# Kernel optimization log

Hardware: AMD Instinct MI355X
Metric: run time of the kernel (lower is better)

The kernel has to match this reference:

```python
import jax, jax.numpy as jnp
import numpy as np

S, B, DIM = 1024, 4, 768
N_EXPERTS = 8
# hidden_dim = 256 * ceil(int(2*4*dim/3)/256) = 2048 for dim=768
HID = 2048


def setup_inputs() -> dict:
    key = jax.random.key(0)
    ks = jax.random.split(key, 6)
    scale = 0.02
    return {
        "hidden_states": jax.random.normal(ks[0], (S, B, DIM), dtype=jnp.float32),
        "router_w": jax.random.normal(ks[1], (DIM, N_EXPERTS), dtype=jnp.float32) * scale,
        "router_b": jnp.zeros((N_EXPERTS,), dtype=jnp.float32),
        "w1": jax.random.normal(ks[2], (N_EXPERTS, DIM, HID), dtype=jnp.float32) * scale,
        "w2": jax.random.normal(ks[3], (N_EXPERTS, DIM, HID), dtype=jnp.float32) * scale,
        "w3": jax.random.normal(ks[4], (N_EXPERTS, HID, DIM), dtype=jnp.float32) * scale,
    }


def reference(hidden_states, router_w, router_b, w1, w2, w3):
    s, b, h = hidden_states.shape
    # top-1 router
    route = jax.nn.softmax(hidden_states @ router_w + router_b, axis=2)  # [s,b,E]
    max_prob = jnp.max(route, axis=2).reshape(-1, 1)   # [T,1]
    max_ind = jnp.argmax(route, axis=2).reshape(-1)    # [T]
    x = hidden_states.reshape(-1, h)                   # [T,d]

    out = jnp.zeros_like(x)
    # fixed small loop over experts; masked dispatch (tokens not routed to e
    # are zeroed so they contribute nothing)
    for e in range(N_EXPERTS):
        mask = (max_ind == e)[:, None]                 # [T,1]
        xe = jnp.where(mask, x, 0.0)
        oe = (jax.nn.silu(xe @ w1[e]) * (xe @ w2[e])) @ w3[e]
        out = out + jnp.where(mask, oe, 0.0)

    # original stores expert outputs in a bf16 buffer before the prob combine
    out = out.astype(jnp.bfloat16) * max_prob          # bf16 * f32 -> f32
    return out.reshape(s, b, h)
```

## Files before the change

kernel.cpp:

```cpp
#include <hip/hip_runtime.h>


#define T_TOK 4096
#define DIM   768
#define HID   2048
#define NE    8
#define ECAP  1024

#define KB1 24
#define NB1 128
#define KB2 64
#define NB2 48
#define MBC 64

typedef _Float16 f16x8 __attribute__((ext_vector_type(8)));
typedef float    f32x4 __attribute__((ext_vector_type(4)));

__device__ __forceinline__ float bf16_rne(float v) {
    unsigned u = __float_as_uint(v);
    unsigned r = (u + 0x7fffu + ((u >> 16) & 1u)) & 0xffff0000u;
    return __uint_as_float(r);
}

__global__ void moe_init_kernel(int* __restrict__ counts) {
    if (threadIdx.x < NE) counts[threadIdx.x] = 0;
}

__global__ __launch_bounds__(256) void moe_convert_kernel(
    const float* __restrict__ w1, const float* __restrict__ w2,
    const float* __restrict__ w3, _Float16* __restrict__ w1s,
    _Float16* __restrict__ w2s, _Float16* __restrict__ w3s)
{
    const int bid = blockIdx.x;
    const float* src; _Float16* dst; int N, KBc, ngrp, kgrp;
    if (bid < 1536) {
        const int e = bid / 192, tile = bid % 192;
        src = w1 + (size_t)e * DIM * HID; dst = w1s + (size_t)e * NB1 * KB1 * 512;
        N = HID; KBc = KB1; ngrp = tile & 15; kgrp = tile >> 4;
    } else if (bid < 3072) {
        const int r = bid - 1536, e = r / 192, tile = r % 192;
        src = w2 + (size_t)e * DIM * HID; dst = w2s + (size_t)e * NB1 * KB1 * 512;
        N = HID; KBc = KB1; ngrp = tile & 15; kgrp = tile >> 4;
    } else {
        const int r = bid - 3072, e = r / 192, tile = r % 192;
        src = w3 + (size_t)e * HID * DIM; dst = w3s + (size_t)e * NB2 * KB2 * 512;
        N = DIM; KBc = KB2; ngrp = tile % 6; kgrp = tile / 6;
    }

    __shared__ float Lt[64 * 130];
    const int t  = threadIdx.x;
    const int c4 = (t & 31) * 4;
    const int r0 = (t >> 5) * 8;
    const float* p = src + (size_t)(kgrp * 64 + r0) * N + ngrp * 128 + c4;
    float4 v[8];
#pragma unroll
    for (int j = 0; j < 8; ++j) v[j] = *(const float4*)(p + (size_t)j * N);
#pragma unroll
    for (int j = 0; j < 8; ++j) {
        float* row = &Lt[(r0 + j) * 130 + c4];
        *(float2*)(row)     = make_float2(v[j].x, v[j].y);
        *(float2*)(row + 2) = make_float2(v[j].z, v[j].w);
    }
    __syncthreads();

    const int l = t & 63, w = t >> 6;
    const int fr = l & 15, fq = l >> 4;
#pragma unroll
    for (int i = 0; i < 4; ++i) {
        const int cell = w * 4 + i;
        const int kbl = cell >> 3, nbl = cell & 7;
        f16x8 h;
#pragma unroll
        for (int j = 0; j < 8; ++j)
            h[j] = (_Float16)Lt[(kbl * 32 + fq * 8 + j) * 130 + nbl * 16 + fr];
        const int nb = ngrp * 8 + nbl, kb = kgrp * 2 + kbl;
        *(f16x8*)(dst + ((size_t)nb * KBc + kb) * 512 + l * 8) = h;
    }
}

__global__ __launch_bounds__(256) void moe_router_kernel(
    const float* __restrict__ X, const float* __restrict__ rw,
    const float* __restrict__ rb, float* __restrict__ probs,
    int* __restrict__ counts, int* __restrict__ lists)
{
    const int t    = blockIdx.x * 4 + (threadIdx.x >> 6);
    const int lane = threadIdx.x & 63;
    const float* x = X + (size_t)t * DIM;

    float xv[12];
#pragma unroll
    for (int j = 0; j < 12; ++j) xv[j] = x[lane + j * 64];

    double lg[NE];
#pragma unroll
    for (int e = 0; e < NE; ++e) {
        double s = 0.0;
#pragma unroll
        for (int j = 0; j < 12; ++j)
            s += (double)xv[j] * (double)rw[(lane + j * 64) * NE + e];
#pragma unroll
        for (int off = 32; off >= 1; off >>= 1) s += __shfl_xor(s, off, 64);
        lg[e] = s + (double)rb[e];
    }

    if (lane == 0) {
        double m = lg[0]; int mi = 0;
#pragma unroll
        for (int e = 1; e < NE; ++e)
            if (lg[e] > m) { m = lg[e]; mi = e; }
        float sum = 0.f;
#pragma unroll
        for (int e = 0; e < NE; ++e) sum += expf((float)(lg[e] - m));
        probs[t] = 1.0f / sum;
        int pos = atomicAdd(&counts[mi], 1);
        lists[mi * T_TOK + pos] = t;
    }
}

__global__ __launch_bounds__(256) void moe_gather_kernel(
    const float* __restrict__ X, const int* __restrict__ lists,
    const int* __restrict__ counts, _Float16* __restrict__ Ag)
{
    const int e = blockIdx.z;
    int cnt = counts[e]; if (cnt > ECAP) cnt = ECAP;
    const int mgrp = blockIdx.y;
    if (mgrp * 64 >= ((cnt + 63) & ~63)) return;
    const int t = threadIdx.x, w = t >> 6, l = t & 63;
    const int mb = mgrp * 4 + w;
    const int m  = mb * 16 + (l & 15);
    const bool valid = (m < cnt);
    const int tok = valid ? lists[e * T_TOK + m] : 0;
    const float* xr = X + (size_t)tok * DIM + (l >> 4) * 8;
#pragma unroll
    for (int i = 0; i < 4; ++i) {
        const int kb = blockIdx.x * 4 + i;
        float4 a = make_float4(0.f, 0.f, 0.f, 0.f), b = a;
        if (valid) {
            a = *(const float4*)(xr + kb * 32);
            b = *(const float4*)(xr + kb * 32 + 4);
        }
        f16x8 h;
        h[0] = (_Float16)a.x; h[1] = (_Float16)a.y; h[2] = (_Float16)a.z; h[3] = (_Float16)a.w;
        h[4] = (_Float16)b.x; h[5] = (_Float16)b.y; h[6] = (_Float16)b.z; h[7] = (_Float16)b.w;
        *(f16x8*)(Ag + ((size_t)(e * MBC + mb) * KB1 + kb) * 512 + l * 8) = h;
    }
}

__global__ __launch_bounds__(256, 3) void moe_gemm1_kernel(
    const _Float16* __restrict__ Ag, const _Float16* __restrict__ w1s,
    const _Float16* __restrict__ w2s, const int* __restrict__ counts,
    _Float16* __restrict__ Hs)
{
    const int e = blockIdx.z;
    int cnt = counts[e]; if (cnt > ECAP) cnt = ECAP;
    const int by = blockIdx.y, bx = blockIdx.x;
    if (by * 128 >= cnt) return;
    const int t = threadIdx.x, w = t >> 6, l = t & 63;
    const int wm = w & 1, wn = w >> 1;

    const _Float16* Ab  = Ag + ((size_t)((e * MBC + by * 8 + wm * 4) * KB1)) * 512 + l * 8;
    const int nb0 = e * NB1 + bx * 4 + wn * 2;
    const _Float16* B1b = w1s + ((size_t)nb0 * KB1) * 512 + l * 8;
    const _Float16* B2b = w2s + ((size_t)nb0 * KB1) * 512 + l * 8;

    f32x4 acc1[4][2], acc2[4][2];
    const f32x4 zero = {0.f, 0.f, 0.f, 0.f};
#pragma unroll
    for (int i = 0; i < 4; ++i)
#pragma unroll
        for (int j = 0; j < 2; ++j) { acc1[i][j] = zero; acc2[i][j] = zero; }

    f16x8 a0[4], p0[2], q0[2], a1[4], p1[2], q1[2];

    auto LD = [&](f16x8* a, f16x8* p, f16x8* q, int kb) {
#pragma unroll
        for (int i = 0; i < 4; ++i)
            a[i] = *(const f16x8*)(Ab + ((size_t)(i * KB1 + kb)) * 512);
#pragma unroll
        for (int j = 0; j < 2; ++j) {
            p[j] = *(const f16x8*)(B1b + ((size_t)(j * KB1 + kb)) * 512);
            q[j] = *(const f16x8*)(B2b + ((size_t)(j * KB1 + kb)) * 512);
        }
    };
    auto FM = [&](const f16x8* a, const f16x8* p, const f16x8* q) {
#pragma unroll
        for (int i = 0; i < 4; ++i)
#pragma unroll
            for (int j = 0; j < 2; ++j) {
                acc1[i][j] = __builtin_amdgcn_mfma_f32_16x16x32_f16(a[i], p[j], acc1[i][j], 0, 0, 0);
                acc2[i][j] = __builtin_amdgcn_mfma_f32_16x16x32_f16(a[i], q[j], acc2[i][j], 0, 0, 0);
            }
    };

    LD(a0, p0, q0, 0);
    int kb = 0;
    for (; kb + 2 < KB1; kb += 2) {
        LD(a1, p1, q1, kb + 1);
        FM(a0, p0, q0);
        LD(a0, p0, q0, kb + 2);
        FM(a1, p1, q1);
    }
    LD(a1, p1, q1, kb + 1);
    FM(a0, p0, q0);
    FM(a1, p1, q1);

    __shared__ _Float16 Ep[4][64 * 40];
    const int fq = l >> 4, fr = l & 15;
#pragma unroll
    for (int i = 0; i < 4; ++i)
#pragma unroll
        for (int j = 0; j < 2; ++j)
#pragma unroll
            for (int r = 0; r < 4; ++r) {
                const float h1 = acc1[i][j][r], h2 = acc2[i][j][r];
                const float s  = h1 / (1.f + __expf(-h1)) * h2;
                Ep[w][(i * 16 + fq * 4 + r) * 40 + j * 16 + fr] = (_Float16)s;
            }
    __syncthreads();
    const int kbH = bx * 2 + wn;
#pragma unroll
    for (int i = 0; i < 4; ++i) {
        f16x8 v = *(const f16x8*)&Ep[w][(i * 16 + fr) * 40 + fq * 8];
        *(f16x8*)(Hs + ((size_t)((e * MBC + by * 8 + wm * 4 + i) * KB2 + kbH)) * 512 + l * 8) = v;
    }
}

__global__ __launch_bounds__(256, 4) void moe_gemm2_kernel(
    const _Float16* __restrict__ Hs, const _Float16* __restrict__ w3s,
    const int* __restrict__ lists, const int* __restrict__ counts,
    const float* __restrict__ probs, float* __restrict__ out)
{
    const int e = blockIdx.z;
    int cnt = counts[e]; if (cnt > ECAP) cnt = ECAP;
    const int by = blockIdx.y, bx = blockIdx.x;
    if (by * 64 >= cnt) return;
    const int t = threadIdx.x, w = t >> 6, l = t & 63;

    const _Float16* Ab = Hs + ((size_t)((e * MBC + by * 4) * KB2)) * 512 + l * 8;
    const int nb0 = e * NB2 + bx * 8 + w * 2;
    const _Float16* Bb = w3s + ((size_t)nb0 * KB2) * 512 + l * 8;

    f32x4 acc[4][2];
    const f32x4 zero = {0.f, 0.f, 0.f, 0.f};
#pragma unroll
    for (int i = 0; i < 4; ++i) { acc[i][0] = zero; acc[i][1] = zero; }

    f16x8 a0[4], b0[2], a1[4], b1[2];

    auto LD = [&](f16x8* a, f16x8* b, int kb) {
#pragma unroll
        for (int i = 0; i < 4; ++i)
            a[i] = *(const f16x8*)(Ab + ((size_t)(i * KB2 + kb)) * 512);
#pragma unroll
        for (int j = 0; j < 2; ++j)
            b[j] = *(const f16x8*)(Bb + ((size_t)(j * KB2 + kb)) * 512);
    };
    auto FM = [&](const f16x8* a, const f16x8* b) {
#pragma unroll
        for (int i = 0; i < 4; ++i)
#pragma unroll
            for (int j = 0; j < 2; ++j)
                acc[i][j] = __builtin_amdgcn_mfma_f32_16x16x32_f16(a[i], b[j], acc[i][j], 0, 0, 0);
    };

    LD(a0, b0, 0);
    int kb = 0;
    for (; kb + 2 < KB2; kb += 2) {
        LD(a1, b1, kb + 1);
        FM(a0, b0);
        LD(a0, b0, kb + 2);
        FM(a1, b1);
    }
    LD(a1, b1, kb + 1);
    FM(a0, b0);
    FM(a1, b1);

    const int* list = lists + e * T_TOK;
    const int fq = l >> 4, fr = l & 15;
    const int c0 = bx * 128 + w * 32;
#pragma unroll
    for (int i = 0; i < 4; ++i)
#pragma unroll
        for (int r = 0; r < 4; ++r) {
            const int m = by * 64 + i * 16 + fq * 4 + r;
            if (m < cnt) {
                const int tok = list[m];
                const float pb = probs[tok];
                float* orow = out + (size_t)tok * DIM + c0 + fr;
                orow[0]  = bf16_rne(acc[i][0][r]) * pb;
                orow[16] = bf16_rne(acc[i][1][r]) * pb;
            }
        }
}

extern "C" void kernel_launch(void* const* d_in, const int* in_sizes, int n_in,
                              void* d_out, int out_size, void* d_ws, size_t ws_size,
                              hipStream_t stream) {
    const float* X  = (const float*)d_in[0];
    const float* rw = (const float*)d_in[1];
    const float* rb = (const float*)d_in[2];
    const float* w1 = (const float*)d_in[3];
    const float* w2 = (const float*)d_in[4];
    const float* w3 = (const float*)d_in[5];
    float* out = (float*)d_out;

    char* ws = (char*)d_ws;
    int*      counts = (int*)(ws + 0);
    int*      lists  = (int*)(ws + 256);
    float*    probs  = (float*)(ws + 131328);
    const size_t WSZ = 25165824;
    _Float16* w1s = (_Float16*)(ws + 147712);
    _Float16* w2s = (_Float16*)(ws + 147712 + WSZ);
    _Float16* w3s = (_Float16*)(ws + 147712 + 2 * WSZ);
    _Float16* Ag  = (_Float16*)(ws + 147712 + 3 * WSZ);
    _Float16* Hs  = (_Float16*)(ws + 147712 + 3 * WSZ + 12582912);

    hipLaunchKernelGGL(moe_init_kernel, dim3(1), dim3(64), 0, stream, counts);
    hipLaunchKernelGGL(moe_convert_kernel, dim3(4608), dim3(256), 0, stream,
                       w1, w2, w3, w1s, w2s, w3s);
    hipLaunchKernelGGL(moe_router_kernel, dim3(T_TOK / 4), dim3(256), 0, stream,
                       X, rw, rb, probs, counts, lists);
    hipLaunchKernelGGL(moe_gather_kernel, dim3(6, 16, 8), dim3(256), 0, stream,
                       X, lists, counts, Ag);
    hipLaunchKernelGGL(moe_gemm1_kernel, dim3(32, 8, 8), dim3(256), 0, stream,
                       Ag, w1s, w2s, counts, Hs);
    hipLaunchKernelGGL(moe_gemm2_kernel, dim3(6, 16, 8), dim3(256), 0, stream,
                       Hs, w3s, lists, counts, probs, out);
}
```

Baseline: 339.9 us.

## Stage GEMM operand fragments through double-buffered LDS with cooperative loads

```diff
diff --git a/kernel.cpp b/kernel.cpp
--- a/kernel.cpp
+++ b/kernel.cpp
@@ -158,10 +158,22 @@
     const int t = threadIdx.x, w = t >> 6, l = t & 63;
     const int wm = w & 1, wn = w >> 1;
 
-    const _Float16* Ab  = Ag + ((size_t)((e * MBC + by * 8 + wm * 4) * KB1)) * 512 + l * 8;
-    const int nb0 = e * NB1 + bx * 4 + wn * 2;
-    const _Float16* B1b = w1s + ((size_t)nb0 * KB1) * 512 + l * 8;
-    const _Float16* B2b = w2s + ((size_t)nb0 * KB1) * 512 + l * 8;
+    __shared__ _Float16 Ls[2][16 * 512];
+    __shared__ _Float16 Ep[4][64 * 40];
+
+    const int c0s = w * 4;
+    const _Float16* gsrc[4];
+#pragma unroll
+    for (int i = 0; i < 4; ++i) {
+        const int c = c0s + i;
+        if (c < 8)
+            gsrc[i] = Ag  + ((size_t)((e * MBC + by * 8 + c) * KB1)) * 512;
+        else if (c < 12)
+            gsrc[i] = w1s + ((size_t)((e * NB1 + bx * 4 + (c - 8)) * KB1)) * 512;
+        else
+            gsrc[i] = w2s + ((size_t)((e * NB1 + bx * 4 + (c - 12)) * KB1)) * 512;
+        gsrc[i] += (size_t)l * 8;
+    }
 
     f32x4 acc1[4][2], acc2[4][2];
     const f32x4 zero = {0.f, 0.f, 0.f, 0.f};
@@ -170,19 +182,31 @@
 #pragma unroll
         for (int j = 0; j < 2; ++j) { acc1[i][j] = zero; acc2[i][j] = zero; }
 
-    f16x8 a0[4], p0[2], q0[2], a1[4], p1[2], q1[2];
-
-    auto LD = [&](f16x8* a, f16x8* p, f16x8* q, int kb) {
+    f16x8 st[4];
+    auto G = [&](int kb) {
 #pragma unroll
         for (int i = 0; i < 4; ++i)
-            a[i] = *(const f16x8*)(Ab + ((size_t)(i * KB1 + kb)) * 512);
+            st[i] = *(const f16x8*)(gsrc[i] + (size_t)kb * 512);
+    };
+
+    G(0);
+    for (int kb = 0; kb < KB1; ++kb) {
+        _Float16* Lb = &Ls[kb & 1][0];
+#pragma unroll
+        for (int i = 0; i < 4; ++i)
+            *(f16x8*)(Lb + (c0s + i) * 512 + l * 8) = st[i];
+        __syncthreads();
+        if (kb + 1 < KB1) G(kb + 1);
+
+        f16x8 a[4], p[2], q[2];
+#pragma unroll
+        for (int i = 0; i < 4; ++i)
+            a[i] = *(const f16x8*)(Lb + (wm * 4 + i) * 512 + l * 8);
 #pragma unroll
         for (int j = 0; j < 2; ++j) {
-            p[j] = *(const f16x8*)(B1b + ((size_t)(j * KB1 + kb)) * 512);
-            q[j] = *(const f16x8*)(B2b + ((size_t)(j * KB1 + kb)) * 512);
+            p[j] = *(const f16x8*)(Lb + (8  + wn * 2 + j) * 512 + l * 8);
+            q[j] = *(const f16x8*)(Lb + (12 + wn * 2 + j) * 512 + l * 8);
         }
-    };
-    auto FM = [&](const f16x8* a, const f16x8* p, const f16x8* q) {
 #pragma unroll
         for (int i = 0; i < 4; ++i)
 #pragma unroll
@@ -190,21 +214,8 @@
                 acc1[i][j] = __builtin_amdgcn_mfma_f32_16x16x32_f16(a[i], p[j], acc1[i][j], 0, 0, 0);
                 acc2[i][j] = __builtin_amdgcn_mfma_f32_16x16x32_f16(a[i], q[j], acc2[i][j], 0, 0, 0);
             }
-    };
-
-    LD(a0, p0, q0, 0);
-    int kb = 0;
-    for (; kb + 2 < KB1; kb += 2) {
-        LD(a1, p1, q1, kb + 1);
-        FM(a0, p0, q0);
-        LD(a0, p0, q0, kb + 2);
-        FM(a1, p1, q1);
-    }
-    LD(a1, p1, q1, kb + 1);
-    FM(a0, p0, q0);
-    FM(a1, p1, q1);
-
-    __shared__ _Float16 Ep[4][64 * 40];
+    }
+
     const int fq = l >> 4, fr = l & 15;
 #pragma unroll
     for (int i = 0; i < 4; ++i)
@@ -225,7 +236,7 @@
     }
 }
 
-__global__ __launch_bounds__(256, 4) void moe_gemm2_kernel(
+__global__ __launch_bounds__(256, 3) void moe_gemm2_kernel(
     const _Float16* __restrict__ Hs, const _Float16* __restrict__ w3s,
     const int* __restrict__ lists, const int* __restrict__ counts,
     const float* __restrict__ probs, float* __restrict__ out)
@@ -236,44 +247,61 @@
     if (by * 64 >= cnt) return;
     const int t = threadIdx.x, w = t >> 6, l = t & 63;
 
-    const _Float16* Ab = Hs + ((size_t)((e * MBC + by * 4) * KB2)) * 512 + l * 8;
-    const int nb0 = e * NB2 + bx * 8 + w * 2;
-    const _Float16* Bb = w3s + ((size_t)nb0 * KB2) * 512 + l * 8;
+    __shared__ _Float16 Ls[2][24 * 512];
+
+    const int c0s = w * 3;
+    const _Float16* gsrc[3];
+#pragma unroll
+    for (int i = 0; i < 3; ++i) {
+        const int c = c0s + i;
+        if (c < 4)
+            gsrc[i] = Hs  + ((size_t)((e * MBC + by * 4 + c) * KB2)) * 512;
+        else
+            gsrc[i] = w3s + ((size_t)((e * NB2 + bx * 8 + (c - 4)) * KB2)) * 512;
+        gsrc[i] += (size_t)l * 8;
+    }
 
     f32x4 acc[4][2];
     const f32x4 zero = {0.f, 0.f, 0.f, 0.f};
 #pragma unroll
     for (int i = 0; i < 4; ++i) { acc[i][0] = zero; acc[i][1] = zero; }
 
-    f16x8 a0[4], b0[2], a1[4], b1[2];
-
-    auto LD = [&](f16x8* a, f16x8* b, int kb) {
-#pragma unroll
-        for (int i = 0; i < 4; ++i)
-            a[i] = *(const f16x8*)(Ab + ((size_t)(i * KB2 + kb)) * 512);
-#pragma unroll
-        for (int j = 0; j < 2; ++j)
-            b[j] = *(const f16x8*)(Bb + ((size_t)(j * KB2 + kb)) * 512);
+    f16x8 st[6];
+    auto G = [&](int kb0) {
+#pragma unroll
+        for (int u = 0; u < 2; ++u)
+#pragma unroll
+            for (int i = 0; i < 3; ++i)
+                st[u * 3 + i] = *(const f16x8*)(gsrc[i] + (size_t)(kb0 + u) * 512);
     };
-    auto FM = [&](const f16x8* a, const f16x8* b) {
-#pragma unroll
-        for (int i = 0; i < 4; ++i)
+
+    G(0);
+    for (int s = 0; s < KB2 / 2; ++s) {
+        _Float16* Lb = &Ls[s & 1][0];
+#pragma unroll
+        for (int u = 0; u < 2; ++u)
+#pragma unroll
+            for (int i = 0; i < 3; ++i)
+                *(f16x8*)(Lb + (u * 12 + c0s + i) * 512 + l * 8) = st[u * 3 + i];
+        __syncthreads();
+        if (s + 1 < KB2 / 2) G(2 * (s + 1));
+
+#pragma unroll
+        for (int u = 0; u < 2; ++u) {
+            f16x8 a[4], b[2];
+#pragma unroll
+            for (int i = 0; i < 4; ++i)
+                a[i] = *(const f16x8*)(Lb + (u * 12 + i) * 512 + l * 8);
 #pragma unroll
             for (int j = 0; j < 2; ++j)
-                acc[i][j] = __builtin_amdgcn_mfma_f32_16x16x32_f16(a[i], b[j], acc[i][j], 0, 0, 0);
-    };
-
-    LD(a0, b0, 0);
-    int kb = 0;
-    for (; kb + 2 < KB2; kb += 2) {
-        LD(a1, b1, kb + 1);
-        FM(a0, b0);
-        LD(a0, b0, kb + 2);
-        FM(a1, b1);
-    }
-    LD(a1, b1, kb + 1);
-    FM(a0, b0);
-    FM(a1, b1);
+                b[j] = *(const f16x8*)(Lb + (u * 12 + 4 + w * 2 + j) * 512 + l * 8);
+#pragma unroll
+            for (int i = 0; i < 4; ++i)
+#pragma unroll
+                for (int j = 0; j < 2; ++j)
+                    acc[i][j] = __builtin_amdgcn_mfma_f32_16x16x32_f16(a[i], b[j], acc[i][j], 0, 0, 0);
+        }
+    }
 
     const int* list = lists + e * T_TOK;
     const int fq = l >> 4, fr = l & 15;
```

Result: faster. 323.3 us (-4.9%).
